# Optimization experiments

Measured on AMD Instinct MI355X. Metric: run time of the kernel, lower is better.

Reference implementation:

```python
import jax, jax.numpy as jnp
import numpy as np

EPS = 1e-6

def setup_inputs() -> dict:
    key = jax.random.key(0)
    k1, k2, k3 = jax.random.split(key, 3)
    B, N, D = 1, 2048, 1024
    x = jax.random.normal(k1, (B, N, D), dtype=jnp.float32)
    W_qvk = jax.random.normal(k2, (D, 3 * D), dtype=jnp.float32) * (D ** -0.5)
    b_qvk = jax.random.normal(k3, (3 * D,), dtype=jnp.float32) * 0.02
    return {"x": x, "W_qvk": W_qvk, "b_qvk": b_qvk, "head_num": 16}


def _forward(x, W_qvk, b_qvk, head_num):
    B, N, D = x.shape
    qvk = x @ W_qvk + b_qvk                       # (B, N, 3D)
    # torch.chunk order in source: q, v, k
    def to_heads(t):
        return t.reshape(B, N, head_num, D // head_num).transpose(0, 2, 1, 3)  # (B,h,N,e)
    q, v, k = (to_heads(t) for t in jnp.split(qvk, 3, axis=-1))
    e = q.shape[-1]
    # causal linear attention, bucket_size=1
    q = jax.nn.softmax(q, axis=-1) * (e ** -0.5)  # (B,h,N,e)
    k = jnp.exp(k)
    k_cumsum = jnp.cumsum(k, axis=2)              # (B,h,N,e)
    # per-position outer product k_i (x) v_i, then causal prefix-sum over N
    kv = jnp.einsum('bhnd,bhne->bhnde', k, v)     # (B,h,N,e,e)
    kv_cumsum = jnp.cumsum(kv, axis=2)            # (B,h,N,e,e)
    denom = jnp.einsum('bhnd,bhnd->bhn', q, k_cumsum + EPS)   # (B,h,N)
    out = jnp.einsum('bhnd,bhnde->bhne', q, kv_cumsum) / denom[..., None]
    # concat heads: (B,h,N,e) -> (B,N,D)
    return out.transpose(0, 2, 1, 3).reshape(B, N, D)


def reference(x, W_qvk, b_qvk, head_num):
    return _forward(x, W_qvk, b_qvk, head_num)
```

## Files before the change

### kernel.cpp

```cpp
#include <hip/hip_runtime.h>
#include <stdint.h>

#define NTOK 2048
#define NCH 32

typedef __attribute__((ext_vector_type(8))) short bf16x8;
typedef __attribute__((ext_vector_type(8))) unsigned short ushort8v;
typedef __attribute__((ext_vector_type(4))) float f32x4;

__device__ __forceinline__ unsigned short f2bf(float f) {
  unsigned u = __float_as_uint(f);
  u += 0x7fffu + ((u >> 16) & 1u);
  return (unsigned short)(u >> 16);
}
__device__ __forceinline__ float bf2f(unsigned short s) {
  return __uint_as_float(((unsigned)s) << 16);
}

__global__ __launch_bounds__(256) void k_prep_inputs(const float* __restrict__ x,
                                                     unsigned short* __restrict__ xb,
                                                     const float* __restrict__ W,
                                                     unsigned short* __restrict__ Wt) {
  int bid = blockIdx.x;
  if (bid < 2048) {
    int i = (bid * 256 + threadIdx.x) * 4;
    float4 v = *(const float4*)(x + i);
    ushort4 o = { f2bf(v.x), f2bf(v.y), f2bf(v.z), f2bf(v.w) };
    *(ushort4*)(xb + i) = o;
  } else {
    __shared__ float tile[32][33];
    int id = bid - 2048;
    int bx = id % 96, by = id / 96;
    int tx = threadIdx.x & 31, ty = threadIdx.x >> 5;
    int c0 = bx * 32;
    int r0 = by * 32;
#pragma unroll
    for (int j = 0; j < 32; j += 8)
      tile[ty + j][tx] = W[(size_t)(r0 + ty + j) * 3072 + c0 + tx];
    __syncthreads();
#pragma unroll
    for (int j = 0; j < 32; j += 8)
      Wt[(size_t)(c0 + ty + j) * 1024 + r0 + tx] = f2bf(tile[tx][ty + j]);
  }
}

__global__ __launch_bounds__(768, 1) void k_gemm_fused(const unsigned short* __restrict__ xb,
                                                       const unsigned short* __restrict__ wt,
                                                       const float* __restrict__ bias,
                                                       unsigned short* __restrict__ qh,
                                                       unsigned short* __restrict__ kh,
                                                       unsigned short* __restrict__ kt,
                                                       unsigned short* __restrict__ vt) {
  __shared__ __align__(16) unsigned short As[3][128][64];
  __shared__ __align__(16) unsigned short Bs[3][192][64];
  const int t = threadIdx.x;
  const int lane = t & 63;
  const int wave = t >> 6;
  const int wr = wave / 3;
  const int wc = wave % 3;
  const int rowBase = blockIdx.y * 128;
  const int colBase = blockIdx.x * 192;
  const int fr = lane & 15;
  const int khalf = lane >> 4;

  const bool isA = t < 256;
  const int nL = isA ? 4 : 3;
  const int bstr = isA ? 16384 : 24576;
  const unsigned short* gsrc[4];
  char* ldst[4];
#pragma unroll
  for (int j = 0; j < 4; ++j) {
    int idx = isA ? (t + j * 256) : (t - 256 + j * 512);
    if (j >= nL) idx = 0;
    int row = idx >> 3;
    int ssl = (idx & 7) ^ (row & 7);
    gsrc[j] = (isA ? xb + (size_t)(rowBase + row) * 1024
                   : wt + (size_t)(colBase + row) * 1024) + ssl * 8;
    ldst[j] = (isA ? (char*)As : (char*)Bs) + idx * 16;
  }

#define STG(buf, kt0) do {                                                                \
    _Pragma("unroll")                                                                     \
    for (int j_ = 0; j_ < 4; ++j_)                                                        \
      if (j_ < nL)                                                                        \
        __builtin_amdgcn_global_load_lds(                                                 \
            (const __attribute__((address_space(1))) void*)(gsrc[j_] + (kt0) * 64),       \
            (__attribute__((address_space(3))) void*)(ldst[j_] + (buf) * bstr), 16, 0, 0);\
  } while (0)

#define VMW_STEADY() do {                                                                 \
    if (isA) asm volatile("s_waitcnt vmcnt(4)" ::: "memory");                             \
    else     asm volatile("s_waitcnt vmcnt(3)" ::: "memory");                             \
  } while (0)
#define VMCNT0() asm volatile("s_waitcnt vmcnt(0)" ::: "memory")
#define LGKM0()  asm volatile("s_waitcnt lgkmcnt(0)" ::: "memory")
#define BAR()    __builtin_amdgcn_s_barrier()

  f32x4 acc[2][4] = {};
  const int fs0 = khalf ^ (fr & 7);

#define LOAD_FRAGS(cur, af, bff) do {                                                     \
    _Pragma("unroll")                                                                     \
    for (int m = 0; m < 2; ++m) {                                                         \
      const unsigned short* r = &As[cur][wr * 32 + m * 16 + fr][0];                       \
      af[m][0] = *(const bf16x8*)(r + fs0 * 8);                                           \
      af[m][1] = *(const bf16x8*)(r + (fs0 ^ 4) * 8);                                     \
    }                                                                                     \
    _Pragma("unroll")                                                                     \
    for (int n = 0; n < 4; ++n) {                                                         \
      const unsigned short* r = &Bs[cur][wc * 64 + n * 16 + fr][0];                       \
      bff[n][0] = *(const bf16x8*)(r + fs0 * 8);                                          \
      bff[n][1] = *(const bf16x8*)(r + (fs0 ^ 4) * 8);                                    \
    }                                                                                     \
  } while (0)

#define DO_MFMA(af, bff) do {                                                             \
    _Pragma("unroll")                                                                     \
    for (int m = 0; m < 2; ++m)                                                           \
      _Pragma("unroll")                                                                   \
      for (int n = 0; n < 4; ++n) {                                                       \
        acc[m][n] = __builtin_amdgcn_mfma_f32_16x16x32_bf16(af[m][0], bff[n][0], acc[m][n], 0, 0, 0); \
        acc[m][n] = __builtin_amdgcn_mfma_f32_16x16x32_bf16(af[m][1], bff[n][1], acc[m][n], 0, 0, 0); \
      }                                                                                   \
  } while (0)

  STG(0, 0);
  STG(1, 1);
#pragma unroll 1
  for (int ktile = 0; ktile < 16; ++ktile) {
    const int cur = ktile % 3;
    if (ktile < 15) { VMW_STEADY(); }
    else            { VMCNT0(); }
    BAR();
    __builtin_amdgcn_sched_barrier(0);
    bf16x8 af[2][2], bff[4][2];
    LOAD_FRAGS(cur, af, bff);
    if (ktile < 14) STG((ktile + 2) % 3, ktile + 2);
    LGKM0();
    __builtin_amdgcn_sched_barrier(0);
    __builtin_amdgcn_s_setprio(1);
    DO_MFMA(af, bff);
    __builtin_amdgcn_s_setprio(0);
  }
#undef STG
#undef LOAD_FRAGS
#undef DO_MFMA

  const int g2 = khalf;
  const int ocol = lane & 15;
  const int col0 = colBase + wc * 64;
  const int region = col0 >> 10;
  const int h = (col0 & 1023) >> 6;
  const int r0 = rowBase + wr * 32;
  const int cch = r0 >> 6;
  const int lbase = (wr & 1) * 32;
  float bv[4];
#pragma unroll
  for (int n = 0; n < 4; ++n) bv[n] = bias[col0 + 16 * n + ocol];

  if (region == 0) {
#pragma unroll
    for (int m = 0; m < 2; ++m) {
#pragma unroll
      for (int i = 0; i < 4; ++i) {
        float v[4];
#pragma unroll
        for (int n = 0; n < 4; ++n) v[n] = acc[m][n][i] + bv[n];
        float mx = fmaxf(fmaxf(v[0], v[1]), fmaxf(v[2], v[3]));
#pragma unroll
        for (int off = 1; off <= 8; off <<= 1) mx = fmaxf(mx, __shfl_xor(mx, off));
        float s = 0.f;
#pragma unroll
        for (int n = 0; n < 4; ++n) { v[n] = __expf(v[n] - mx); s += v[n]; }
#pragma unroll
        for (int off = 1; off <= 8; off <<= 1) s += __shfl_xor(s, off);
        float inv = 0.125f / s;
        int tok = r0 + 16 * m + 4 * g2 + i;
        unsigned short* qrow = qh + ((size_t)h * NTOK + tok) * 64;
#pragma unroll
        for (int n = 0; n < 4; ++n) qrow[16 * n + ocol] = f2bf(v[n] * inv);
      }
    }
  } else if (region == 1) {
    unsigned short* vb = vt + (size_t)(h * NCH + cch) * 4096;
#pragma unroll
    for (int m = 0; m < 2; ++m) {
      int tl = lbase + 16 * m + 4 * g2;
#pragma unroll
      for (int n = 0; n < 4; ++n) {
        int e = 16 * n + ocol;
        ushort4 p = { f2bf(acc[m][n][0] + bv[n]), f2bf(acc[m][n][1] + bv[n]),
                      f2bf(acc[m][n][2] + bv[n]), f2bf(acc[m][n][3] + bv[n]) };
        *(ushort4*)&vb[(size_t)e * 64 + tl] = p;
      }
    }
  } else {
    unsigned short* kb = kt + (size_t)(h * NCH + cch) * 4096;
#pragma unroll
    for (int m = 0; m < 2; ++m) {
      int tl = lbase + 16 * m + 4 * g2;
#pragma unroll
      for (int n = 0; n < 4; ++n) {
        int e = 16 * n + ocol;
        float kv[4];
#pragma unroll
        for (int i = 0; i < 4; ++i) kv[i] = __expf(acc[m][n][i] + bv[n]);
        ushort4 p = { f2bf(kv[0]), f2bf(kv[1]), f2bf(kv[2]), f2bf(kv[3]) };
        *(ushort4*)&kb[(size_t)e * 64 + tl] = p;
#pragma unroll
        for (int i = 0; i < 4; ++i)
          kh[((size_t)h * NTOK + r0 + 16 * m + 4 * g2 + i) * 64 + e] = p[i];
      }
    }
  }
}

__global__ __launch_bounds__(256) void k_chunk_sums(const unsigned short* __restrict__ kt,
                                                    const unsigned short* __restrict__ vt,
                                                    unsigned short* __restrict__ Sc,
                                                    float* __restrict__ zc) {
  int h = blockIdx.x >> 5, c = blockIdx.x & 31;
  __shared__ __align__(16) unsigned short Kt[64][72], Vt[64][72];
  int t = threadIdx.x, lane = t & 63, w = t >> 6;
  int fr = lane & 15, g = lane >> 4, fko = g * 8;
  const unsigned short* kg = kt + (size_t)(h * NCH + c) * 4096;
  const unsigned short* vg = vt + (size_t)(h * NCH + c) * 4096;
  for (int s = t; s < 512; s += 256) {
    int r = s >> 3, c8 = (s & 7) * 8;
    *(ushort8v*)&Kt[r][c8] = *(const ushort8v*)&kg[r * 64 + c8];
    *(ushort8v*)&Vt[r][c8] = *(const ushort8v*)&vg[r * 64 + c8];
  }
  __syncthreads();
  bf16x8 ka[2];
#pragma unroll
  for (int ks = 0; ks < 2; ++ks) ka[ks] = *(const bf16x8*)&Kt[16 * w + fr][32 * ks + fko];
  f32x4 s4[4] = {};
#pragma unroll
  for (int nb = 0; nb < 4; ++nb)
#pragma unroll
    for (int ks = 0; ks < 2; ++ks) {
      bf16x8 vf = *(const bf16x8*)&Vt[16 * nb + fr][32 * ks + fko];
      s4[nb] = __builtin_amdgcn_mfma_f32_16x16x32_bf16(ka[ks], vf, s4[nb], 0, 0, 0);
    }
  unsigned short* so = Sc + (size_t)(h * NCH + c) * 4096;
#pragma unroll
  for (int nb = 0; nb < 4; ++nb) {
    ushort4 o = { f2bf(s4[nb][0]), f2bf(s4[nb][1]), f2bf(s4[nb][2]), f2bf(s4[nb][3]) };
    *(ushort4*)&so[(size_t)(16 * nb + fr) * 64 + 16 * w + 4 * g] = o;
  }
  if (w == 0) {
    float z = 0.f;
#pragma unroll
    for (int j = 0; j < 8; ++j) {
      bf16x8 kv = *(const bf16x8*)&Kt[lane][j * 8];
#pragma unroll
      for (int e = 0; e < 8; ++e) z += bf2f((unsigned short)kv[e]);
    }
    zc[(size_t)(h * NCH + c) * 64 + lane] = z;
  }
}

__global__ __launch_bounds__(256) void k_scan(const unsigned short* __restrict__ Sc,
                                              unsigned short* __restrict__ Sp,
                                              const float* __restrict__ zc,
                                              float* __restrict__ zp) {
  int b = blockIdx.x;
  if (b < 256) {
    int tg = b * 256 + threadIdx.x;
    int h = tg >> 12, e = tg & 4095;
    float run = 0.f;
    for (int c = 0; c < NCH; ++c) {
      size_t idx = (size_t)(h * NCH + c) * 4096 + e;
      float v = bf2f(Sc[idx]);
      Sp[idx] = f2bf(run);
      run += v;
    }
  } else {
#pragma unroll
    for (int j = 0; j < 4; ++j) {
      int s = threadIdx.x + j * 256;
      int h = s >> 6, d = s & 63;
      float run = 0.f;
      for (int c = 0; c < NCH; ++c) {
        size_t idx = (size_t)(h * NCH + c) * 64 + d;
        zp[idx] = run;
        run += zc[idx];
      }
    }
  }
}

__global__ __launch_bounds__(256) void k_attn(const unsigned short* __restrict__ qh,
                                              const unsigned short* __restrict__ kh,
                                              const unsigned short* __restrict__ vt,
                                              const unsigned short* __restrict__ Sp,
                                              const float* __restrict__ zp,
                                              float* __restrict__ out) {
  int h = blockIdx.x >> 5, c = blockIdx.x & 31;
  __shared__ __align__(16) unsigned short Qs[64][72], Ks[64][72], Vts[64][72], Sts[64][72], Ams[64][72];
  __shared__ __align__(16) float zs[64];
  __shared__ float denom[64];
  int t = threadIdx.x, lane = t & 63, w = t >> 6;
  int fr = lane & 15, g = lane >> 4, fko = g * 8;
  const unsigned short* qg = qh + ((size_t)h * NTOK + c * 64) * 64;
  const unsigned short* kg = kh + ((size_t)h * NTOK + c * 64) * 64;
  const unsigned short* vg = vt + (size_t)(h * NCH + c) * 4096;
  const unsigned short* sg = Sp + (size_t)(h * NCH + c) * 4096;
  for (int s = t; s < 512; s += 256) {
    int r = s >> 3, c8 = (s & 7) * 8;
    *(ushort8v*)&Qs[r][c8]  = *(const ushort8v*)&qg[r * 64 + c8];
    *(ushort8v*)&Ks[r][c8]  = *(const ushort8v*)&kg[r * 64 + c8];
    *(ushort8v*)&Vts[r][c8] = *(const ushort8v*)&vg[r * 64 + c8];
    *(ushort8v*)&Sts[r][c8] = *(const ushort8v*)&sg[r * 64 + c8];
  }
  if (t < 64) zs[t] = zp[(size_t)(h * NCH + c) * 64 + t];
  __syncthreads();

  bf16x8 qa[2];
#pragma unroll
  for (int ks = 0; ks < 2; ++ks) qa[ks] = *(const bf16x8*)&Qs[16 * w + fr][32 * ks + fko];
  f32x4 a1[4] = {};
#pragma unroll
  for (int mb = 0; mb < 4; ++mb)
#pragma unroll
    for (int ks = 0; ks < 2; ++ks) {
      bf16x8 kf = *(const bf16x8*)&Ks[16 * mb + fr][32 * ks + fko];
      a1[mb] = __builtin_amdgcn_mfma_f32_16x16x32_bf16(qa[ks], kf, a1[mb], 0, 0, 0);
    }
#pragma unroll
  for (int i = 0; i < 4; ++i) {
    int n = 16 * w + 4 * g + i;
    ushort4 qv4 = *(const ushort4*)&Qs[n][fr * 4];
    float4  zv4 = *(const float4*)&zs[fr * 4];
    float rs = bf2f(qv4.x) * zv4.x + bf2f(qv4.y) * zv4.y +
               bf2f(qv4.z) * zv4.z + bf2f(qv4.w) * zv4.w;
#pragma unroll
    for (int mb = 0; mb < 4; ++mb) {
      int m = 16 * mb + fr;
      float v = (m <= n) ? a1[mb][i] : 0.f;
      a1[mb][i] = v;
      rs += v;
      Ams[n][16 * mb + fr] = f2bf(v);
    }
#pragma unroll
    for (int off = 1; off <= 8; off <<= 1) rs += __shfl_xor(rs, off);
    if (fr == 0) denom[n] = rs + 1.25e-7f;
  }
  __syncthreads();

  bf16x8 xa[4];
#pragma unroll
  for (int ks = 0; ks < 2; ++ks) {
    xa[ks]     = *(const bf16x8*)&Vts[16 * w + fr][32 * ks + fko];
    xa[2 + ks] = *(const bf16x8*)&Sts[16 * w + fr][32 * ks + fko];
  }
  f32x4 o4[4] = {};
#pragma unroll
  for (int nb = 0; nb < 4; ++nb)
#pragma unroll
    for (int ks = 0; ks < 2; ++ks) {
      bf16x8 afr = *(const bf16x8*)&Ams[16 * nb + fr][32 * ks + fko];
      o4[nb] = __builtin_amdgcn_mfma_f32_16x16x32_bf16(xa[ks], afr, o4[nb], 0, 0, 0);
      bf16x8 qfr = *(const bf16x8*)&Qs[16 * nb + fr][32 * ks + fko];
      o4[nb] = __builtin_amdgcn_mfma_f32_16x16x32_bf16(xa[2 + ks], qfr, o4[nb], 0, 0, 0);
    }
#pragma unroll
  for (int nb = 0; nb < 4; ++nb) {
    int n = 16 * nb + fr;
    float dv = denom[n];
    float4 res = { o4[nb][0] / dv, o4[nb][1] / dv, o4[nb][2] / dv, o4[nb][3] / dv };
    *(float4*)&out[(size_t)(c * 64 + n) * 1024 + h * 64 + 16 * w + 4 * g] = res;
  }
}

extern "C" void kernel_launch(void* const* d_in, const int* in_sizes, int n_in,
                              void* d_out, int out_size, void* d_ws, size_t ws_size,
                              hipStream_t stream) {
  (void)in_sizes; (void)n_in; (void)out_size; (void)ws_size;
  const float* x = (const float*)d_in[0];
  const float* W = (const float*)d_in[1];
  const float* b = (const float*)d_in[2];
  char* ws = (char*)d_ws;

  const size_t MB = 1024 * 1024;
  unsigned short* xb = (unsigned short*)(ws + 0);
  unsigned short* Wt = (unsigned short*)(ws + 4 * MB);
  unsigned short* qh = (unsigned short*)(ws + 10 * MB);
  unsigned short* kh = (unsigned short*)(ws + 14 * MB);
  unsigned short* kt = (unsigned short*)(ws + 18 * MB);
  unsigned short* vt = (unsigned short*)(ws + 22 * MB);
  unsigned short* Sc = (unsigned short*)(ws + 26 * MB);
  unsigned short* Sp = (unsigned short*)(ws + 30 * MB);
  float*          zc = (float*)(ws + 34 * MB);
  float*          zp = (float*)(ws + 34 * MB + 131072);

  k_prep_inputs<<<dim3(5120), dim3(256), 0, stream>>>(x, xb, W, Wt);
  k_gemm_fused<<<dim3(16, 16), dim3(768), 0, stream>>>(xb, Wt, b, qh, kh, kt, vt);
  k_chunk_sums<<<dim3(512), dim3(256), 0, stream>>>(kt, vt, Sc, zc);
  k_scan<<<dim3(257), dim3(256), 0, stream>>>(Sc, Sp, zc, zp);
  k_attn<<<dim3(512), dim3(256), 0, stream>>>(qh, kh, vt, Sp, zp, (float*)d_out);
}
```

Before: 46.33 us.

## Fuse per-chunk KV sums into QKV GEMM epilogue via permuted weight layout

The transposed weight matrix is written in a permuted column order so that each GEMM block's 192 columns hold q, v and k for a single head. With that layout the GEMM epilogue can stage exp(k) and v tiles in the reused A-tile shared memory and compute the per-chunk K^T V sums and k column sums directly. This removes the separate chunk-sums kernel launch and the global round trip of the transposed k buffer. In exchange the epilogue gets longer, with extra barriers and only 8 of 12 waves doing the MFMA work.

```diff
diff --git a/kernel.cpp b/kernel.cpp
--- a/kernel.cpp
+++ b/kernel.cpp
@@ -39,8 +39,11 @@
       tile[ty + j][tx] = W[(size_t)(r0 + ty + j) * 3072 + c0 + tx];
     __syncthreads();
 #pragma unroll
-    for (int j = 0; j < 32; j += 8)
-      Wt[(size_t)(c0 + ty + j) * 1024 + r0 + tx] = f2bf(tile[tx][ty + j]);
+    for (int j = 0; j < 32; j += 8) {
+      int oc = c0 + ty + j;
+      int rowp = ((oc & 1023) >> 6) * 192 + (oc >> 10) * 64 + (oc & 63);
+      Wt[(size_t)rowp * 1024 + r0 + tx] = f2bf(tile[tx][ty + j]);
+    }
   }
 }
 
@@ -49,8 +52,9 @@
                                                        const float* __restrict__ bias,
                                                        unsigned short* __restrict__ qh,
                                                        unsigned short* __restrict__ kh,
-                                                       unsigned short* __restrict__ kt,
-                                                       unsigned short* __restrict__ vt) {
+                                                       unsigned short* __restrict__ vt,
+                                                       unsigned short* __restrict__ Sc,
+                                                       float* __restrict__ zc) {
   __shared__ __align__(16) unsigned short As[3][128][64];
   __shared__ __align__(16) unsigned short Bs[3][192][64];
   const int t = threadIdx.x;
@@ -146,17 +150,21 @@
 #undef LOAD_FRAGS
 #undef DO_MFMA
 
+  BAR();
+  unsigned short (*Lkv)[2][64][72] =
+      reinterpret_cast<unsigned short (*)[2][64][72]>(&As[0][0][0]);
+
   const int g2 = khalf;
   const int ocol = lane & 15;
-  const int col0 = colBase + wc * 64;
-  const int region = col0 >> 10;
-  const int h = (col0 & 1023) >> 6;
+  const int region = wc;
+  const int h = blockIdx.x;
   const int r0 = rowBase + wr * 32;
   const int cch = r0 >> 6;
+  const int cq = wr >> 1;
   const int lbase = (wr & 1) * 32;
   float bv[4];
 #pragma unroll
-  for (int n = 0; n < 4; ++n) bv[n] = bias[col0 + 16 * n + ocol];
+  for (int n = 0; n < 4; ++n) bv[n] = bias[region * 1024 + h * 64 + 16 * n + ocol];
 
   if (region == 0) {
 #pragma unroll
@@ -192,10 +200,10 @@
         ushort4 p = { f2bf(acc[m][n][0] + bv[n]), f2bf(acc[m][n][1] + bv[n]),
                       f2bf(acc[m][n][2] + bv[n]), f2bf(acc[m][n][3] + bv[n]) };
         *(ushort4*)&vb[(size_t)e * 64 + tl] = p;
+        *(ushort4*)&Lkv[cq][1][e][tl] = p;
       }
     }
   } else {
-    unsigned short* kb = kt + (size_t)(h * NCH + cch) * 4096;
 #pragma unroll
     for (int m = 0; m < 2; ++m) {
       int tl = lbase + 16 * m + 4 * g2;
@@ -206,57 +214,47 @@
 #pragma unroll
         for (int i = 0; i < 4; ++i) kv[i] = __expf(acc[m][n][i] + bv[n]);
         ushort4 p = { f2bf(kv[0]), f2bf(kv[1]), f2bf(kv[2]), f2bf(kv[3]) };
-        *(ushort4*)&kb[(size_t)e * 64 + tl] = p;
+        *(ushort4*)&Lkv[cq][0][e][tl] = p;
 #pragma unroll
         for (int i = 0; i < 4; ++i)
           kh[((size_t)h * NTOK + r0 + 16 * m + 4 * g2 + i) * 64 + e] = p[i];
       }
     }
   }
-}
-
-__global__ __launch_bounds__(256) void k_chunk_sums(const unsigned short* __restrict__ kt,
-                                                    const unsigned short* __restrict__ vt,
-                                                    unsigned short* __restrict__ Sc,
-                                                    float* __restrict__ zc) {
-  int h = blockIdx.x >> 5, c = blockIdx.x & 31;
-  __shared__ __align__(16) unsigned short Kt[64][72], Vt[64][72];
-  int t = threadIdx.x, lane = t & 63, w = t >> 6;
-  int fr = lane & 15, g = lane >> 4, fko = g * 8;
-  const unsigned short* kg = kt + (size_t)(h * NCH + c) * 4096;
-  const unsigned short* vg = vt + (size_t)(h * NCH + c) * 4096;
-  for (int s = t; s < 512; s += 256) {
-    int r = s >> 3, c8 = (s & 7) * 8;
-    *(ushort8v*)&Kt[r][c8] = *(const ushort8v*)&kg[r * 64 + c8];
-    *(ushort8v*)&Vt[r][c8] = *(const ushort8v*)&vg[r * 64 + c8];
-  }
-  __syncthreads();
-  bf16x8 ka[2];
-#pragma unroll
-  for (int ks = 0; ks < 2; ++ks) ka[ks] = *(const bf16x8*)&Kt[16 * w + fr][32 * ks + fko];
-  f32x4 s4[4] = {};
-#pragma unroll
-  for (int nb = 0; nb < 4; ++nb)
-#pragma unroll
-    for (int ks = 0; ks < 2; ++ks) {
-      bf16x8 vf = *(const bf16x8*)&Vt[16 * nb + fr][32 * ks + fko];
-      s4[nb] = __builtin_amdgcn_mfma_f32_16x16x32_bf16(ka[ks], vf, s4[nb], 0, 0, 0);
-    }
-  unsigned short* so = Sc + (size_t)(h * NCH + c) * 4096;
-#pragma unroll
-  for (int nb = 0; nb < 4; ++nb) {
-    ushort4 o = { f2bf(s4[nb][0]), f2bf(s4[nb][1]), f2bf(s4[nb][2]), f2bf(s4[nb][3]) };
-    *(ushort4*)&so[(size_t)(16 * nb + fr) * 64 + 16 * w + 4 * g] = o;
-  }
-  if (w == 0) {
-    float z = 0.f;
-#pragma unroll
-    for (int j = 0; j < 8; ++j) {
-      bf16x8 kv = *(const bf16x8*)&Kt[lane][j * 8];
-#pragma unroll
-      for (int e = 0; e < 8; ++e) z += bf2f((unsigned short)kv[e]);
-    }
-    zc[(size_t)(h * NCH + c) * 64 + lane] = z;
+  BAR();
+
+  if (wave < 8) {
+    const int q = wave >> 2;
+    const int w4 = wave & 3;
+    const int cchg = 2 * blockIdx.y + q;
+    bf16x8 ka[2];
+#pragma unroll
+    for (int ks = 0; ks < 2; ++ks)
+      ka[ks] = *(const bf16x8*)&Lkv[q][0][16 * w4 + fr][32 * ks + khalf * 8];
+    f32x4 s4[4] = {};
+#pragma unroll
+    for (int nb = 0; nb < 4; ++nb)
+#pragma unroll
+      for (int ks = 0; ks < 2; ++ks) {
+        bf16x8 vf = *(const bf16x8*)&Lkv[q][1][16 * nb + fr][32 * ks + khalf * 8];
+        s4[nb] = __builtin_amdgcn_mfma_f32_16x16x32_bf16(ka[ks], vf, s4[nb], 0, 0, 0);
+      }
+    unsigned short* so = Sc + (size_t)(h * NCH + cchg) * 4096;
+#pragma unroll
+    for (int nb = 0; nb < 4; ++nb) {
+      ushort4 o = { f2bf(s4[nb][0]), f2bf(s4[nb][1]), f2bf(s4[nb][2]), f2bf(s4[nb][3]) };
+      *(ushort4*)&so[(size_t)(16 * nb + fr) * 64 + 16 * w4 + 4 * g2] = o;
+    }
+    if (w4 == 0) {
+      float z = 0.f;
+#pragma unroll
+      for (int j = 0; j < 8; ++j) {
+        bf16x8 kv = *(const bf16x8*)&Lkv[q][0][lane][j * 8];
+#pragma unroll
+        for (int e = 0; e < 8; ++e) z += bf2f((unsigned short)kv[e]);
+      }
+      zc[(size_t)(h * NCH + cchg) * 64 + lane] = z;
+    }
   }
 }
 
@@ -313,7 +311,7 @@
     *(ushort8v*)&Vts[r][c8] = *(const ushort8v*)&vg[r * 64 + c8];
     *(ushort8v*)&Sts[r][c8] = *(const ushort8v*)&sg[r * 64 + c8];
   }
-  if (t < 64) zs[t] = zp[(size_t)(h * NCH + c) * 64 + t];
+  if (t < 64) zs[t] = zp[(size_t)h * NCH * 64 + (size_t)c * 64 + t];
   __syncthreads();
 
   bf16x8 qa[2];
@@ -387,16 +385,14 @@
   unsigned short* Wt = (unsigned short*)(ws + 4 * MB);
   unsigned short* qh = (unsigned short*)(ws + 10 * MB);
   unsigned short* kh = (unsigned short*)(ws + 14 * MB);
-  unsigned short* kt = (unsigned short*)(ws + 18 * MB);
-  unsigned short* vt = (unsigned short*)(ws + 22 * MB);
-  unsigned short* Sc = (unsigned short*)(ws + 26 * MB);
-  unsigned short* Sp = (unsigned short*)(ws + 30 * MB);
-  float*          zc = (float*)(ws + 34 * MB);
-  float*          zp = (float*)(ws + 34 * MB + 131072);
+  unsigned short* vt = (unsigned short*)(ws + 18 * MB);
+  unsigned short* Sc = (unsigned short*)(ws + 22 * MB);
+  unsigned short* Sp = (unsigned short*)(ws + 26 * MB);
+  float*          zc = (float*)(ws + 30 * MB);
+  float*          zp = (float*)(ws + 30 * MB + 131072);
 
   k_prep_inputs<<<dim3(5120), dim3(256), 0, stream>>>(x, xb, W, Wt);
-  k_gemm_fused<<<dim3(16, 16), dim3(768), 0, stream>>>(xb, Wt, b, qh, kh, kt, vt);
-  k_chunk_sums<<<dim3(512), dim3(256), 0, stream>>>(kt, vt, Sc, zc);
+  k_gemm_fused<<<dim3(16, 16), dim3(768), 0, stream>>>(xb, Wt, b, qh, kh, vt, Sc, zc);
   k_scan<<<dim3(257), dim3(256), 0, stream>>>(Sc, Sp, zc, zp);
   k_attn<<<dim3(512), dim3(256), 0, stream>>>(qh, kh, vt, Sp, zp, (float*)d_out);
 }
```

New measurement: 44.17 us, median of 3. -4.7%, faster.
